# Optimization experiments

Hardware: AMD Instinct MI355X
Metric: run time of the kernel (lower is better)

## Reference

```python
import jax, jax.numpy as jnp
import numpy as np

BLOCK_SIZES = [256] * 16
LAYER_SIZE = sum(BLOCK_SIZES)  # 4096
N_ROWS = 8192


def _block_diag_mask(sizes):
    m = np.zeros((sum(sizes), sum(sizes)), dtype=bool)
    off = 0
    for s in sizes:
        m[off:off + s, off:off + s] = True
        off += s
    return jnp.asarray(m)


def setup_inputs() -> dict:
    key = jax.random.key(0)
    k1, k2 = jax.random.split(key)
    mask = _block_diag_mask(BLOCK_SIZES)
    # _blocks param: block_diagonal(raw_blocks) -> dense matrix, zero off-block
    blocks = jax.random.normal(k1, (LAYER_SIZE, LAYER_SIZE), dtype=jnp.float32) * mask
    x = jax.random.normal(k2, (N_ROWS, LAYER_SIZE), dtype=jnp.float32)
    return {"x": x, "blocks": blocks, "mask": mask}


def reference(x, blocks, mask):
    # blocks property: mask then tanh (constrained='tanh'); tanh(0)=0 preserves structure
    b = jnp.tanh(blocks * mask)
    # forward: dense matmul x @ blocks (no bias)
    return x @ b
```

## Files before the change

### kernel.cpp

```cpp
#include <hip/hip_runtime.h>
#include <stdint.h>


typedef float floatx4 __attribute__((ext_vector_type(4)));
typedef __bf16 bf16x8 __attribute__((ext_vector_type(8)));

#define LDX 4096
#define NBLK 16
#define BS 256
#define BM 64
#define BN 256
#define BK 32

__device__ __forceinline__ unsigned int f2bf(float f) {
  union { float f; unsigned int i; } x;
  x.f = f;
  unsigned int r = x.i + 0x7FFFu + ((x.i >> 16) & 1u);
  return r >> 16;
}

__device__ __forceinline__ void async_copy16(const void* g, void* l) {
  __builtin_amdgcn_global_load_lds(
      (__attribute__((address_space(1))) void*)(uintptr_t)g,
      (__attribute__((address_space(3))) void*)(unsigned int)(uintptr_t)l,
      16, 0, 0);
}

__global__ __launch_bounds__(256) void tanh_pack(const float* __restrict__ blocks,
                                                 unsigned short* __restrict__ wsT) {
  __shared__ float tile[64][65];
  const int t = threadIdx.x;
  const int tc = blockIdx.x, tr = blockIdx.y, j = blockIdx.z;
  const float* src = blocks + (size_t)(j * BS + tr * 64) * LDX + j * BS + tc * 64;
#pragma unroll
  for (int it = 0; it < 8; ++it) {
    int v = it * 256 + t;
    int row = v >> 5;
    int c2 = (v & 31) * 2;
    float2 f = *(const float2*)(src + (size_t)row * LDX + c2);
    tile[row][c2] = tanhf(f.x);
    tile[row][c2 + 1] = tanhf(f.y);
  }
  __syncthreads();
  unsigned short* dst = wsT + (size_t)j * BS * BS + (size_t)(tc * 64) * BS + tr * 64;
#pragma unroll
  for (int it = 0; it < 8; ++it) {
    int v = it * 256 + t;
    int nn = v >> 5;
    int k2 = (v & 31) * 2;
    unsigned int pair = f2bf(tile[k2][nn]) | (f2bf(tile[k2 + 1][nn]) << 16);
    *(unsigned int*)(dst + (size_t)nn * BS + k2) = pair;
  }
}

template <int BSTR, bool FUSED>
__global__ __launch_bounds__(256) void bdgemm(const float* __restrict__ x,
                                              const void* __restrict__ bsrc,
                                              float* __restrict__ out) {
  __shared__ unsigned short As[BM * BK];
  __shared__ unsigned short Bs[BN * BSTR];
  const int t = threadIdx.x;
  const int lane = t & 63;
  const int wave = t >> 6;
  const int mtile = blockIdx.x;
  const int j = blockIdx.y;
  const int m0 = mtile * BM;

  const float* xg = x + (size_t)m0 * LDX + j * BS;

  const int srow = t >> 2;
  const int scol = (t & 3) * 8;
  const int wn = wave * 64;
  const int fr = lane & 15;
  const int fq = (lane >> 4) * 8;

  floatx4 acc[4][4];
#pragma unroll
  for (int a = 0; a < 4; ++a)
#pragma unroll
    for (int b = 0; b < 4; ++b) acc[a][b] = (floatx4){0.f, 0.f, 0.f, 0.f};

  for (int kt = 0; kt < 8; ++kt) {
    const int k0 = kt * BK;
    const float* ap = xg + (size_t)srow * LDX + k0 + scol;
    float4 a0 = *(const float4*)(ap);
    float4 a1 = *(const float4*)(ap + 4);
    uint4 pk;
    pk.x = f2bf(a0.x) | (f2bf(a0.y) << 16);
    pk.y = f2bf(a0.z) | (f2bf(a0.w) << 16);
    pk.z = f2bf(a1.x) | (f2bf(a1.y) << 16);
    pk.w = f2bf(a1.z) | (f2bf(a1.w) << 16);
    *(uint4*)(As + t * 8) = pk;

    if constexpr (!FUSED) {
      const unsigned short* wsb =
          (const unsigned short*)bsrc + (size_t)j * BS * BS;
#pragma unroll
      for (int i = 0; i < 4; ++i) {
        const int n = i * 64 + (t >> 2);
        async_copy16(wsb + (size_t)n * BS + k0 + scol, Bs + i * 2048 + t * 8);
      }
    } else {
      const float* bg = (const float*)bsrc;
#pragma unroll
      for (int i = 0; i < 32; ++i) {
        const int idx = i * 256 + t;
        const int kk = idx >> 8;
        const int nn = idx & 255;
        float v = tanhf(bg[(size_t)(j * BS + k0 + kk) * LDX + j * BS + nn]);
        Bs[nn * BSTR + kk] = (unsigned short)f2bf(v);
      }
    }
    __syncthreads();

    bf16x8 af[4], bfm[4];
#pragma unroll
    for (int i = 0; i < 4; ++i) {
      af[i] = *(const bf16x8*)(As + (i * 16 + fr) * BK + fq);
      bfm[i] = *(const bf16x8*)(Bs + (wn + i * 16 + fr) * BSTR + fq);
    }
#pragma unroll
    for (int mi = 0; mi < 4; ++mi)
#pragma unroll
      for (int ni = 0; ni < 4; ++ni)
        acc[mi][ni] =
            __builtin_amdgcn_mfma_f32_16x16x32_bf16(af[mi], bfm[ni], acc[mi][ni], 0, 0, 0);
    __syncthreads();
  }

  const int r0 = (lane >> 4) * 4;
  const int ocol = j * BS + wn + fr;
#pragma unroll
  for (int mi = 0; mi < 4; ++mi)
#pragma unroll
    for (int ni = 0; ni < 4; ++ni) {
      float* op = out + (size_t)(m0 + mi * 16 + r0) * LDX + ocol + ni * 16;
#pragma unroll
      for (int r = 0; r < 4; ++r) op[(size_t)r * LDX] = acc[mi][ni][r];
    }
}

extern "C" void kernel_launch(void* const* d_in, const int* in_sizes, int n_in,
                              void* d_out, int out_size, void* d_ws, size_t ws_size,
                              hipStream_t stream) {
  const float* x = (const float*)d_in[0];
  const float* blocks = (const float*)d_in[1];
  float* out = (float*)d_out;

  const size_t need = (size_t)NBLK * BS * BS * sizeof(unsigned short);
  dim3 grid(128, NBLK);
  if (d_ws != nullptr && ws_size >= need) {
    unsigned short* wsT = (unsigned short*)d_ws;
    tanh_pack<<<dim3(4, 4, NBLK), 256, 0, stream>>>(blocks, wsT);
    bdgemm<BK, false><<<grid, 256, 0, stream>>>(x, wsT, out);
  } else {
    bdgemm<40, true><<<grid, 256, 0, stream>>>(x, blocks, out);
  }
}
```

Baseline: 318.2 us.

## Keep full 256x256 weight block resident in LDS and stream A from registers

```diff
diff --git a/kernel.cpp b/kernel.cpp
--- a/kernel.cpp
+++ b/kernel.cpp
@@ -8,9 +8,6 @@
 #define LDX 4096
 #define NBLK 16
 #define BS 256
-#define BM 64
-#define BN 256
-#define BK 32
 
 __device__ __forceinline__ unsigned int f2bf(float f) {
   union { float f; unsigned int i; } x;
@@ -19,12 +16,28 @@
   return r >> 16;
 }
 
+__device__ __forceinline__ bf16x8 pack8(const float4& a, const float4& b) {
+  union { uint4 u; bf16x8 h; } v;
+  v.u.x = f2bf(a.x) | (f2bf(a.y) << 16);
+  v.u.y = f2bf(a.z) | (f2bf(a.w) << 16);
+  v.u.z = f2bf(b.x) | (f2bf(b.y) << 16);
+  v.u.w = f2bf(b.z) | (f2bf(b.w) << 16);
+  return v.h;
+}
+
 __device__ __forceinline__ void async_copy16(const void* g, void* l) {
   __builtin_amdgcn_global_load_lds(
       (__attribute__((address_space(1))) void*)(uintptr_t)g,
       (__attribute__((address_space(3))) void*)(unsigned int)(uintptr_t)l,
       16, 0, 0);
 }
+
+#define BWAIT(N)                                              \
+  do {                                                        \
+    asm volatile("s_waitcnt vmcnt(" #N ")" ::: "memory");     \
+    __builtin_amdgcn_s_barrier();                             \
+    __builtin_amdgcn_sched_barrier(0);                        \
+  } while (0)
 
 __global__ __launch_bounds__(256) void tanh_pack(const float* __restrict__ blocks,
                                                  unsigned short* __restrict__ wsT) {
@@ -42,32 +55,123 @@
     tile[row][c2 + 1] = tanhf(f.y);
   }
   __syncthreads();
-  unsigned short* dst = wsT + (size_t)j * BS * BS + (size_t)(tc * 64) * BS + tr * 64;
+  unsigned char* dstj =
+      (unsigned char*)wsT + (size_t)j * 131072 + (size_t)tr * 32768;
 #pragma unroll
   for (int it = 0; it < 8; ++it) {
     int v = it * 256 + t;
     int nn = v >> 5;
     int k2 = (v & 31) * 2;
+    int n = tc * 64 + nn;
     unsigned int pair = f2bf(tile[k2][nn]) | (f2bf(tile[k2 + 1][nn]) << 16);
-    *(unsigned int*)(dst + (size_t)nn * BS + k2) = pair;
-  }
-}
-
-template <int BSTR, bool FUSED>
-__global__ __launch_bounds__(256) void bdgemm(const float* __restrict__ x,
-                                              const void* __restrict__ bsrc,
-                                              float* __restrict__ out) {
-  __shared__ unsigned short As[BM * BK];
-  __shared__ unsigned short Bs[BN * BSTR];
+    unsigned int off = (unsigned)n * 128 + (((unsigned)(k2 * 2)) ^ (((unsigned)(n & 7)) << 4));
+    *(unsigned int*)(dstj + off) = pair;
+  }
+}
+
+__global__ __launch_bounds__(512, 2) void bdgemm2(const float* __restrict__ x,
+                                                  const unsigned short* __restrict__ wsT,
+                                                  float* __restrict__ out) {
+  __shared__ unsigned short Bs[65536];
+  const int t = threadIdx.x;
+  const int lane = t & 63;
+  const int wave = t >> 6;
+  const int mg = blockIdx.x;
+  const int j = blockIdx.y;
+
+  const int fr = lane & 15;
+  const int kq = lane >> 4;
+  const int sw = (fr & 7) << 4;
+  const int ko0 = ((kq * 16) + 0) ^ sw;
+  const int ko1 = ((kq * 16) + 64) ^ sw;
+
+  const float* xg = x + (size_t)(mg * 512 + wave * 32 + fr) * LDX + j * BS + kq * 8;
+  char* ldsb = (char*)Bs;
+
+  float4 s0[8], s1[8];
+  floatx4 acc[2][16];
+
+  auto issueA = [&](float4* s, int sc) {
+#pragma unroll
+    for (int kt = 0; kt < 2; ++kt)
+#pragma unroll
+      for (int mi = 0; mi < 2; ++mi) {
+        const float* q = xg + (size_t)((sc >> 2) * 256 + mi * 16) * LDX +
+                         (sc & 3) * 64 + kt * 32;
+        s[kt * 4 + mi * 2 + 0] = *(const float4*)(q);
+        s[kt * 4 + mi * 2 + 1] = *(const float4*)(q + 4);
+      }
+  };
+
+  auto compute = [&](int c, const float4* s) {
+#pragma unroll
+    for (int kt = 0; kt < 2; ++kt) {
+      bf16x8 af0 = pack8(s[kt * 4 + 0], s[kt * 4 + 1]);
+      bf16x8 af1 = pack8(s[kt * 4 + 2], s[kt * 4 + 3]);
+      const char* bkt = ldsb + c * 32768 + fr * 128 + (kt ? ko1 : ko0);
+#pragma unroll
+      for (int ni = 0; ni < 16; ++ni) {
+        bf16x8 bf = *(const bf16x8*)(bkt + ni * 2048);
+        acc[0][ni] = __builtin_amdgcn_mfma_f32_16x16x32_bf16(af0, bf, acc[0][ni], 0, 0, 0);
+        acc[1][ni] = __builtin_amdgcn_mfma_f32_16x16x32_bf16(af1, bf, acc[1][ni], 0, 0, 0);
+      }
+    }
+  };
+
+  auto zacc = [&]() {
+#pragma unroll
+    for (int a = 0; a < 2; ++a)
+#pragma unroll
+      for (int b = 0; b < 16; ++b) acc[a][b] = (floatx4){0.f, 0.f, 0.f, 0.f};
+  };
+
+  auto store = [&](int mblk) {
+    float* op = out + (size_t)(mg * 512 + mblk * 256 + wave * 32 + kq * 4) * LDX +
+                j * BS + fr;
+#pragma unroll
+    for (int mi = 0; mi < 2; ++mi)
+#pragma unroll
+      for (int ni = 0; ni < 16; ++ni)
+#pragma unroll
+        for (int r = 0; r < 4; ++r)
+          op[(size_t)(mi * 16 + r) * LDX + ni * 16] = acc[mi][ni][r];
+  };
+
+  issueA(s0, 0);
+  issueA(s1, 1);
+  const char* wsj = (const char*)wsT + (size_t)j * 131072;
+#pragma unroll
+  for (int i = 0; i < 16; ++i)
+    async_copy16(wsj + i * 8192 + t * 16, ldsb + i * 8192 + t * 16);
+
+  zacc();
+  BWAIT(12); compute(0, s0); issueA(s0, 2);
+  BWAIT(16); compute(1, s1); issueA(s1, 3);
+  BWAIT(20); compute(2, s0); issueA(s0, 4);
+  BWAIT(24); compute(3, s1); issueA(s1, 5);
+  store(0);
+
+  zacc();
+  compute(0, s0); issueA(s0, 6);
+  compute(1, s1); issueA(s1, 7);
+  compute(2, s0);
+  compute(3, s1);
+  store(1);
+}
+
+template <int BSTR>
+__global__ __launch_bounds__(256) void bdgemm_fused(const float* __restrict__ x,
+                                                    const float* __restrict__ bg,
+                                                    float* __restrict__ out) {
+  __shared__ unsigned short As[64 * 32];
+  __shared__ unsigned short Bsf[256 * BSTR];
   const int t = threadIdx.x;
   const int lane = t & 63;
   const int wave = t >> 6;
   const int mtile = blockIdx.x;
   const int j = blockIdx.y;
-  const int m0 = mtile * BM;
-
+  const int m0 = mtile * 64;
   const float* xg = x + (size_t)m0 * LDX + j * BS;
-
   const int srow = t >> 2;
   const int scol = (t & 3) * 8;
   const int wn = wave * 64;
@@ -81,7 +185,7 @@
     for (int b = 0; b < 4; ++b) acc[a][b] = (floatx4){0.f, 0.f, 0.f, 0.f};
 
   for (int kt = 0; kt < 8; ++kt) {
-    const int k0 = kt * BK;
+    const int k0 = kt * 32;
     const float* ap = xg + (size_t)srow * LDX + k0 + scol;
     float4 a0 = *(const float4*)(ap);
     float4 a1 = *(const float4*)(ap + 4);
@@ -91,33 +195,20 @@
     pk.z = f2bf(a1.x) | (f2bf(a1.y) << 16);
     pk.w = f2bf(a1.z) | (f2bf(a1.w) << 16);
     *(uint4*)(As + t * 8) = pk;
-
-    if constexpr (!FUSED) {
-      const unsigned short* wsb =
-          (const unsigned short*)bsrc + (size_t)j * BS * BS;
-#pragma unroll
-      for (int i = 0; i < 4; ++i) {
-        const int n = i * 64 + (t >> 2);
-        async_copy16(wsb + (size_t)n * BS + k0 + scol, Bs + i * 2048 + t * 8);
-      }
-    } else {
-      const float* bg = (const float*)bsrc;
-#pragma unroll
-      for (int i = 0; i < 32; ++i) {
-        const int idx = i * 256 + t;
-        const int kk = idx >> 8;
-        const int nn = idx & 255;
-        float v = tanhf(bg[(size_t)(j * BS + k0 + kk) * LDX + j * BS + nn]);
-        Bs[nn * BSTR + kk] = (unsigned short)f2bf(v);
-      }
+#pragma unroll
+    for (int i = 0; i < 32; ++i) {
+      const int idx = i * 256 + t;
+      const int kk = idx >> 8;
+      const int nn = idx & 255;
+      float v = tanhf(bg[(size_t)(j * BS + k0 + kk) * LDX + j * BS + nn]);
+      Bsf[nn * BSTR + kk] = (unsigned short)f2bf(v);
     }
     __syncthreads();
-
     bf16x8 af[4], bfm[4];
 #pragma unroll
     for (int i = 0; i < 4; ++i) {
-      af[i] = *(const bf16x8*)(As + (i * 16 + fr) * BK + fq);
-      bfm[i] = *(const bf16x8*)(Bs + (wn + i * 16 + fr) * BSTR + fq);
+      af[i] = *(const bf16x8*)(As + (i * 16 + fr) * 32 + fq);
+      bfm[i] = *(const bf16x8*)(Bsf + (wn + i * 16 + fr) * BSTR + fq);
     }
 #pragma unroll
     for (int mi = 0; mi < 4; ++mi)
@@ -127,7 +218,6 @@
             __builtin_amdgcn_mfma_f32_16x16x32_bf16(af[mi], bfm[ni], acc[mi][ni], 0, 0, 0);
     __syncthreads();
   }
-
   const int r0 = (lane >> 4) * 4;
   const int ocol = j * BS + wn + fr;
 #pragma unroll
@@ -148,12 +238,11 @@
   float* out = (float*)d_out;
 
   const size_t need = (size_t)NBLK * BS * BS * sizeof(unsigned short);
-  dim3 grid(128, NBLK);
   if (d_ws != nullptr && ws_size >= need) {
     unsigned short* wsT = (unsigned short*)d_ws;
     tanh_pack<<<dim3(4, 4, NBLK), 256, 0, stream>>>(blocks, wsT);
-    bdgemm<BK, false><<<grid, 256, 0, stream>>>(x, wsT, out);
+    bdgemm2<<<dim3(16, NBLK), 512, 0, stream>>>(x, wsT, out);
   } else {
-    bdgemm<40, true><<<grid, 256, 0, stream>>>(x, blocks, out);
-  }
-}
+    bdgemm_fused<40><<<dim3(128, NBLK), 256, 0, stream>>>(x, blocks, out);
+  }
+}
```

Measured after the change: 307.7 us. -3.3%, faster.
